# Optimization experiments

Measured on AMD Instinct MI355X. Metric: run time of the kernel, lower is better.

## Reference

```python
import jax, jax.numpy as jnp
import numpy as np

VEC_DIM = 128
N_DOCS = 1_000_000
N_WORDS = 100_000
B = 16384
C = 8   # context window size
S = 10  # negative samples


def setup_inputs() -> dict:
    key = jax.random.key(0)
    k1, k2, k3, k4, k5 = jax.random.split(key, 5)
    doc_ids = jax.random.randint(k1, (B,), 0, N_DOCS, dtype=jnp.int64) if jax.config.jax_enable_x64 else jax.random.randint(k1, (B,), 0, N_DOCS, dtype=jnp.int32)
    context_ids = jax.random.randint(k2, (B, C), 0, N_WORDS, dtype=jnp.int32)
    sample_ids = jax.random.randint(k3, (B, S), 0, N_WORDS, dtype=jnp.int32)
    paragraph_matrix = jax.random.normal(k4, (N_DOCS, VEC_DIM), dtype=jnp.float32)
    word_matrix = jax.random.normal(k5, (N_WORDS, VEC_DIM), dtype=jnp.float32)
    outputs = jnp.zeros((VEC_DIM, N_WORDS), dtype=jnp.float32)
    return {
        "doc_ids": doc_ids,
        "context_ids": context_ids,
        "sample_ids": sample_ids,
        "paragraph_matrix": paragraph_matrix,
        "word_matrix": word_matrix,
        "outputs": outputs,
    }


def reference(doc_ids, context_ids, sample_ids, paragraph_matrix, word_matrix, outputs):
    # inputs = P[doc] + sum_c W[context]  -> [B, D]
    inputs = paragraph_matrix[doc_ids] + jnp.sum(word_matrix[context_ids], axis=1)
    # outputs[:, sample_ids] -> gather columns; equivalent to outputs.T[sample_ids] -> [B, S, D]
    out_vecs = outputs.T[sample_ids]
    # bmm([B,1,D] @ [B,D,S]) -> [B, S]
    return jnp.einsum("bd,bsd->bs", inputs, out_vecs)
```

## Files before the change

kernel.cpp:

```cpp
#include <hip/hip_runtime.h>


#define VEC_DIM 128
#define NW      100000
#define NW4     (NW / 4)
#define CTX     8
#define NSAMP   10
#define TWB     32
#define TS      132

__global__ __launch_bounds__(256) void transpose_kernel(
    const float* __restrict__ in,
    float* __restrict__ outT)
{
    __shared__ float tile[TWB * TS];
    const int t  = threadIdx.x;
    const int w0 = blockIdx.x * TWB;

    const float4* __restrict__ in4 = (const float4*)in;
    #pragma unroll
    for (int i = 0; i < 4; ++i) {
        const int f4i = i * 256 + t;
        const int d = f4i >> 3;
        const int u = f4i & 7;
        float4 v = in4[d * NW4 + (w0 >> 2) + u];
        tile[(4 * u + 0) * TS + d] = v.x;
        tile[(4 * u + 1) * TS + d] = v.y;
        tile[(4 * u + 2) * TS + d] = v.z;
        tile[(4 * u + 3) * TS + d] = v.w;
    }
    __syncthreads();

    float4* __restrict__ outT4 = (float4*)outT;
    const float4* tile4 = (const float4*)tile;
    #pragma unroll
    for (int i = 0; i < 4; ++i) {
        const int f4i = i * 256 + t;
        const int w = f4i >> 5;
        const int q = f4i & 31;
        outT4[(w0 + w) * 32 + q] = tile4[w * 33 + q];
    }
}

__global__ __launch_bounds__(256) void dm_fwd_kernel(
    const int* __restrict__ doc_ids,
    const int* __restrict__ context_ids,
    const int* __restrict__ sample_ids,
    const float* __restrict__ P,
    const float* __restrict__ W,
    const float* __restrict__ outsT,
    float* __restrict__ out)
{
    const int t = threadIdx.x & 31;
    const int b = blockIdx.x * 8 + (threadIdx.x >> 5);

    const float4* __restrict__ P4 = (const float4*)P;
    const float4* __restrict__ W4 = (const float4*)W;
    const float4* __restrict__ O4 = (const float4*)outsT;

    float4 v = P4[doc_ids[b] * 32 + t];
    #pragma unroll
    for (int c = 0; c < CTX; ++c) {
        float4 w4 = W4[context_ids[b * CTX + c] * 32 + t];
        v.x += w4.x; v.y += w4.y; v.z += w4.z; v.w += w4.w;
    }

    int wids[NSAMP];
    #pragma unroll
    for (int s = 0; s < NSAMP; ++s) wids[s] = sample_ids[b * NSAMP + s];

    #pragma unroll
    for (int s = 0; s < NSAMP; ++s) {
        float4 o = O4[wids[s] * 32 + t];
        float p = v.x * o.x + v.y * o.y + v.z * o.z + v.w * o.w;
        #pragma unroll
        for (int off = 16; off > 0; off >>= 1)
            p += __shfl_down(p, off, 32);
        if (t == 0) out[b * NSAMP + s] = p;
    }
}

__global__ __launch_bounds__(128) void dm_fwd_direct(
    const int* __restrict__ doc_ids,
    const int* __restrict__ context_ids,
    const int* __restrict__ sample_ids,
    const float* __restrict__ P,
    const float* __restrict__ W,
    const float* __restrict__ outs,
    float* __restrict__ out)
{
    const int b = blockIdx.x;
    const int d = threadIdx.x;
    const int lane = d & 63;
    const int wave = d >> 6;

    float v = P[(long)doc_ids[b] * VEC_DIM + d];
    #pragma unroll
    for (int c = 0; c < CTX; ++c)
        v += W[(long)context_ids[b * CTX + c] * VEC_DIM + d];

    __shared__ float partial[2 * NSAMP];
    #pragma unroll
    for (int s = 0; s < NSAMP; ++s) {
        const int w = sample_ids[b * NSAMP + s];
        float p = v * outs[(long)d * NW + w];
        #pragma unroll
        for (int off = 32; off > 0; off >>= 1)
            p += __shfl_down(p, off, 64);
        if (lane == 0) partial[wave * NSAMP + s] = p;
    }
    __syncthreads();
    if (d < NSAMP) out[b * NSAMP + d] = partial[d] + partial[NSAMP + d];
}

extern "C" void kernel_launch(void* const* d_in, const int* in_sizes, int n_in,
                              void* d_out, int out_size, void* d_ws, size_t ws_size,
                              hipStream_t stream) {
    const int*   doc_ids     = (const int*)d_in[0];
    const int*   context_ids = (const int*)d_in[1];
    const int*   sample_ids  = (const int*)d_in[2];
    const float* P           = (const float*)d_in[3];
    const float* W           = (const float*)d_in[4];
    const float* outs        = (const float*)d_in[5];
    float*       out         = (float*)d_out;

    const int B = in_sizes[0];
    const size_t needed = (size_t)NW * VEC_DIM * sizeof(float);

    if (ws_size >= needed) {
        float* outsT = (float*)d_ws;
        transpose_kernel<<<NW / TWB, 256, 0, stream>>>(outs, outsT);
        dm_fwd_kernel<<<B / 8, 256, 0, stream>>>(doc_ids, context_ids, sample_ids,
                                                 P, W, outsT, out);
    } else {
        dm_fwd_direct<<<B, 128, 0, stream>>>(doc_ids, context_ids, sample_ids,
                                             P, W, outs, out);
    }
}
```

Before: 43.84 us.

## Fuse transpose and lookup into one cooperative kernel with grid sync

Merges the transpose of the output matrix and the embedding gather/dot stage into a single cooperative kernel of 2048 blocks. Each block first gathers its input vectors, then transposes a strided share of the tiles, does a grid-wide sync, and computes the dot products. The aim is to remove one kernel launch and overlap the gather latency with the transpose. In exchange it adds a grid barrier and an occupancy query on every call, and it drops the fallback path that ran when the workspace was too small.

```diff
diff --git a/kernel.cpp b/kernel.cpp
--- a/kernel.cpp
+++ b/kernel.cpp
@@ -1,4 +1,7 @@
 #include <hip/hip_runtime.h>
+#include <hip/hip_cooperative_groups.h>
+
+namespace cg = cooperative_groups;
 
 
 #define VEC_DIM 128
@@ -8,10 +11,81 @@
 #define NSAMP   10
 #define TWB     32
 #define TS      132
+#define NTILES  (NW / TWB)
+#define COOP_GRID 2048
+
+__global__ __launch_bounds__(256, 8) void dm_fused_coop(
+    const int* __restrict__ doc_ids,
+    const int* __restrict__ context_ids,
+    const int* __restrict__ sample_ids,
+    const float* __restrict__ P,
+    const float* __restrict__ W,
+    const float* __restrict__ outs,
+    float* __restrict__ outsT,
+    float* __restrict__ out)
+{
+    __shared__ float tile[TWB * TS];
+    const int t    = threadIdx.x;
+    const int tsub = t & 31;
+    const int b    = blockIdx.x * 8 + (t >> 5);
+
+    const float4* __restrict__ P4 = (const float4*)P;
+    const float4* __restrict__ W4 = (const float4*)W;
+    float4 v = P4[doc_ids[b] * 32 + tsub];
+    #pragma unroll
+    for (int c = 0; c < CTX; ++c) {
+        float4 w4 = W4[context_ids[b * CTX + c] * 32 + tsub];
+        v.x += w4.x; v.y += w4.y; v.z += w4.z; v.w += w4.w;
+    }
+
+    const float4* __restrict__ in4 = (const float4*)outs;
+    float4* __restrict__ outT4 = (float4*)outsT;
+    for (int ti = blockIdx.x; ti < NTILES; ti += COOP_GRID) {
+        const int w0 = ti * TWB;
+        __syncthreads();
+        #pragma unroll
+        for (int i = 0; i < 4; ++i) {
+            const int f4i = i * 256 + t;
+            const int d = f4i >> 3;
+            const int u = f4i & 7;
+            float4 x = in4[d * NW4 + (w0 >> 2) + u];
+            tile[(4 * u + 0) * TS + d] = x.x;
+            tile[(4 * u + 1) * TS + d] = x.y;
+            tile[(4 * u + 2) * TS + d] = x.z;
+            tile[(4 * u + 3) * TS + d] = x.w;
+        }
+        __syncthreads();
+        const float4* tile4 = (const float4*)tile;
+        #pragma unroll
+        for (int i = 0; i < 4; ++i) {
+            const int f4i = i * 256 + t;
+            const int w = f4i >> 5;
+            const int q = f4i & 31;
+            outT4[(w0 + w) * 32 + q] = tile4[w * 33 + q];
+        }
+    }
+
+    __threadfence();
+    cg::this_grid().sync();
+
+    const float4* __restrict__ O4 = (const float4*)outsT;
+    int wids[NSAMP];
+    #pragma unroll
+    for (int s = 0; s < NSAMP; ++s) wids[s] = sample_ids[b * NSAMP + s];
+
+    #pragma unroll
+    for (int s = 0; s < NSAMP; ++s) {
+        float4 o = O4[wids[s] * 32 + tsub];
+        float p = v.x * o.x + v.y * o.y + v.z * o.z + v.w * o.w;
+        #pragma unroll
+        for (int off = 16; off > 0; off >>= 1)
+            p += __shfl_down(p, off, 32);
+        if (tsub == 0) out[b * NSAMP + s] = p;
+    }
+}
 
 __global__ __launch_bounds__(256) void transpose_kernel(
-    const float* __restrict__ in,
-    float* __restrict__ outT)
+    const float* __restrict__ in, float* __restrict__ outT)
 {
     __shared__ float tile[TWB * TS];
     const int t  = threadIdx.x;
@@ -30,7 +104,6 @@
         tile[(4 * u + 3) * TS + d] = v.w;
     }
     __syncthreads();
-
     float4* __restrict__ outT4 = (float4*)outT;
     const float4* tile4 = (const float4*)tile;
     #pragma unroll
@@ -80,60 +153,43 @@
     }
 }
 
-__global__ __launch_bounds__(128) void dm_fwd_direct(
-    const int* __restrict__ doc_ids,
-    const int* __restrict__ context_ids,
-    const int* __restrict__ sample_ids,
-    const float* __restrict__ P,
-    const float* __restrict__ W,
-    const float* __restrict__ outs,
-    float* __restrict__ out)
-{
-    const int b = blockIdx.x;
-    const int d = threadIdx.x;
-    const int lane = d & 63;
-    const int wave = d >> 6;
-
-    float v = P[(long)doc_ids[b] * VEC_DIM + d];
-    #pragma unroll
-    for (int c = 0; c < CTX; ++c)
-        v += W[(long)context_ids[b * CTX + c] * VEC_DIM + d];
-
-    __shared__ float partial[2 * NSAMP];
-    #pragma unroll
-    for (int s = 0; s < NSAMP; ++s) {
-        const int w = sample_ids[b * NSAMP + s];
-        float p = v * outs[(long)d * NW + w];
-        #pragma unroll
-        for (int off = 32; off > 0; off >>= 1)
-            p += __shfl_down(p, off, 64);
-        if (lane == 0) partial[wave * NSAMP + s] = p;
-    }
-    __syncthreads();
-    if (d < NSAMP) out[b * NSAMP + d] = partial[d] + partial[NSAMP + d];
-}
-
 extern "C" void kernel_launch(void* const* d_in, const int* in_sizes, int n_in,
                               void* d_out, int out_size, void* d_ws, size_t ws_size,
                               hipStream_t stream) {
-    const int*   doc_ids     = (const int*)d_in[0];
-    const int*   context_ids = (const int*)d_in[1];
-    const int*   sample_ids  = (const int*)d_in[2];
-    const float* P           = (const float*)d_in[3];
-    const float* W           = (const float*)d_in[4];
-    const float* outs        = (const float*)d_in[5];
-    float*       out         = (float*)d_out;
+    const int* doc_ids     = (const int*)d_in[0];
+    const int* context_ids = (const int*)d_in[1];
+    const int* sample_ids  = (const int*)d_in[2];
+    const float* P         = (const float*)d_in[3];
+    const float* W         = (const float*)d_in[4];
+    const float* outs      = (const float*)d_in[5];
+    float* out             = (float*)d_out;
 
     const int B = in_sizes[0];
     const size_t needed = (size_t)NW * VEC_DIM * sizeof(float);
+    float* outsT = (float*)d_ws;
+
+    bool coop_ok = (ws_size >= needed) && (B == 16384);
+    if (coop_ok) {
+        int max_blocks_per_cu = 0;
+        hipError_t qerr = hipOccupancyMaxActiveBlocksPerMultiprocessor(
+            &max_blocks_per_cu, (const void*)dm_fused_coop, 256, 0);
+        if (qerr != hipSuccess || max_blocks_per_cu < 8) coop_ok = false;
+    }
+
+    if (coop_ok) {
+        void* args[] = {
+            (void*)&doc_ids, (void*)&context_ids, (void*)&sample_ids,
+            (void*)&P, (void*)&W, (void*)&outs, (void*)&outsT, (void*)&out
+        };
+        hipError_t lerr = hipLaunchCooperativeKernel(
+            (const void*)dm_fused_coop, dim3(COOP_GRID), dim3(256),
+            args, 0, stream);
+        if (lerr == hipSuccess) return;
+    }
 
     if (ws_size >= needed) {
-        float* outsT = (float*)d_ws;
         transpose_kernel<<<NW / TWB, 256, 0, stream>>>(outs, outsT);
         dm_fwd_kernel<<<B / 8, 256, 0, stream>>>(doc_ids, context_ids, sample_ids,
                                                  P, W, outsT, out);
-    } else {
-        dm_fwd_direct<<<B, 128, 0, stream>>>(doc_ids, context_ids, sample_ids,
-                                             P, W, outs, out);
     }
 }
```

Result: no change. 44.20 us (+0.8%).
